# Kernel optimization log

Hardware: AMD Instinct MI355X
Metric: run time of the kernel (lower is better)

The kernel has to match this reference:

```python
import jax, jax.numpy as jnp
import numpy as np

B, N, D = 8, 65536, 3
K = 64                 # num_centers
NPOINT = 4096
M = NPOINT // K * 2    # max_neighbors = 128
S = NPOINT // K        # fps samples per group = 64
NITER = 10             # KMeans default Niter


def _sqdist(src, dst):
    # ||s||^2 + ||d||^2 - 2 s.d   (same math as (s-d)^2 sum, GEMM form)
    s2 = (src ** 2).sum(-1)[:, :, None]          # [B,N,1]
    d2 = (dst ** 2).sum(-1)[:, None, :]          # [B,1,K]
    return s2 + d2 - 2.0 * jnp.einsum('bnd,bkd->bnk', src, dst)


def _kmeans(x):
    Bb, Nn, Dd = x.shape
    c = x[:, :K, :]
    bidx = jnp.arange(Bb)[:, None]               # broadcast with cl [B,N]
    for _ in range(NITER):
        cl = jnp.argmin(_sqdist(x, c), axis=2)   # [B,N] cluster codes
        c = jnp.zeros((Bb, K, Dd), x.dtype).at[bidx, cl].add(x)
        ncl = jnp.zeros((Bb, K), x.dtype).at[bidx, cl].add(1.0)
        c = c / ncl[:, :, None]
    return c


def _query_neighbor(x, centers):
    dist = _sqdist(x, centers)                   # [B,N,K]
    negd = -jnp.transpose(dist, (0, 2, 1))       # [B,K,N]
    _, nidx = jax.lax.top_k(negd, M)             # M nearest points per center
    bidx = jnp.arange(x.shape[0])[:, None, None]
    return x[bidx, nidx]                         # [B,K,M,3]


def _batch_fps(xyz, farthest0):
    # xyz: [B,G,Nn,3]; sequential farthest-point sampling per group
    Bb, G, Nn, _ = xyz.shape
    dist0 = jnp.full((Bb, G, Nn), 1e10, xyz.dtype)

    def step(carry, _):
        distance, farthest = carry
        centroid = jnp.take_along_axis(xyz, farthest[:, :, None, None], axis=2)  # [B,G,1,3]
        d = ((xyz - centroid) ** 2).sum(-1)       # [B,G,Nn]
        distance = jnp.minimum(distance, d)
        new_far = jnp.argmax(distance, -1).astype(farthest.dtype)
        return (distance, new_far), farthest      # store index BEFORE update

    _, idx = jax.lax.scan(step, (dist0, farthest0), None, length=S)
    idx = jnp.transpose(idx, (1, 2, 0))           # [B,G,S]
    idx3 = jnp.broadcast_to(idx[..., None], idx.shape + (3,))
    new_xyz = jnp.take_along_axis(xyz, idx3, axis=2)  # [B,G,S,3]
    return new_xyz.reshape(Bb, G * S, 3)


def setup_inputs() -> dict:
    key = jax.random.key(0)
    k1, k2 = jax.random.split(key)
    x = jax.random.normal(k1, (B, N, D), dtype=jnp.float32)
    farthest0 = jax.random.randint(k2, (B, K), 0, M, dtype=jnp.int32)
    return {"x": x, "farthest0": farthest0}


def reference(x, farthest0):
    centers = _kmeans(x)                  # [B,K,3]
    neighbor = _query_neighbor(x, centers)  # [B,K,M,3]
    new_xyz = _batch_fps(neighbor, farthest0)  # [B, NPOINT, 3]
    return new_xyz, centers
```

## Files before the change

### kernel.cpp

```cpp
#include <hip/hip_runtime.h>
#include <stdint.h>

#pragma clang fp contract(off)

#define B 8
#define N 65536
#define KC 64
#define M 128
#define S 64
#define NITER 10
#define NWAVES 16
#define HPAD 257
#define SAMPLE 8192
#define SCAP 2048
#define CAPG 3072
#define WCAP 512
#define CSTRIDE 32
#define UPD_T 1024
#define RANGE 16384
#define NRANGE (N / RANGE)
#define PPT (RANGE / UPD_T)
#define GBATCH 2048

using u32 = unsigned int;
using u64 = unsigned long long;

__device__ __forceinline__ float sq3(float a, float b, float c) {
  return __fadd_rn(__fadd_rn(__fmul_rn(a, a), __fmul_rn(b, b)), __fmul_rn(c, c));
}
__device__ __forceinline__ float dot3(float x0, float x1, float x2,
                                      float c0, float c1, float c2) {
  return __fadd_rn(__fadd_rn(__fmul_rn(x0, c0), __fmul_rn(x1, c1)), __fmul_rn(x2, c2));
}
__device__ __forceinline__ float distf(float s2, float d2, float dt) {
  return __fsub_rn(__fadd_rn(s2, d2), __fmul_rn(2.0f, dt));
}
__device__ __forceinline__ u32 fkey(float f) {
  u32 u = __float_as_uint(f);
  return (u & 0x80000000u) ? ~u : (u | 0x80000000u);
}


__global__ void k_init_centers(const float* __restrict__ x, float* __restrict__ centers) {
  int i = blockIdx.x * blockDim.x + threadIdx.x;
  if (i >= B * KC * 3) return;
  int b = i / (KC * 3);
  int r = i % (KC * 3);
  centers[i] = x[(size_t)b * N * 3 + r];
}

__global__ __launch_bounds__(256)
void k_assign(const float* __restrict__ x, const float* __restrict__ centers,
              unsigned char* __restrict__ cl) {
  __shared__ float4 cs[KC];
  int g = blockIdx.x;
  int b = g & 7;
  int chunk = g >> 3;
  int t = threadIdx.x;
  if (t < KC) {
    float a0 = centers[(b * KC + t) * 3 + 0];
    float a1 = centers[(b * KC + t) * 3 + 1];
    float a2 = centers[(b * KC + t) * 3 + 2];
    cs[t] = make_float4(a0, a1, a2, sq3(a0, a1, a2));
  }
  __syncthreads();
  int q = chunk * 256 + t;
  const float4* xb4 = (const float4*)(x + (size_t)b * N * 3);
  float4 A = xb4[3 * q], Bv = xb4[3 * q + 1], C = xb4[3 * q + 2];
  float p0x = A.x, p0y = A.y, p0z = A.z;
  float p1x = A.w, p1y = Bv.x, p1z = Bv.y;
  float p2x = Bv.z, p2y = Bv.w, p2z = C.x;
  float p3x = C.y, p3y = C.z, p3z = C.w;
  float s0 = sq3(p0x, p0y, p0z);
  float s1 = sq3(p1x, p1y, p1z);
  float s2 = sq3(p2x, p2y, p2z);
  float s3 = sq3(p3x, p3y, p3z);
  float inf = __int_as_float(0x7f800000);
  float b0 = inf, b1 = inf, b2 = inf, b3 = inf;
  int i0 = 0, i1 = 0, i2 = 0, i3 = 0;
  for (int k = 0; k < KC; ++k) {
    float4 cc = cs[k];
    float d0 = distf(s0, cc.w, dot3(p0x, p0y, p0z, cc.x, cc.y, cc.z));
    float d1 = distf(s1, cc.w, dot3(p1x, p1y, p1z, cc.x, cc.y, cc.z));
    float d2 = distf(s2, cc.w, dot3(p2x, p2y, p2z, cc.x, cc.y, cc.z));
    float d3 = distf(s3, cc.w, dot3(p3x, p3y, p3z, cc.x, cc.y, cc.z));
    if (d0 < b0) { b0 = d0; i0 = k; }
    if (d1 < b1) { b1 = d1; i1 = k; }
    if (d2 < b2) { b2 = d2; i2 = k; }
    if (d3 < b3) { b3 = d3; i3 = k; }
  }
  *(u32*)(cl + (size_t)b * N + 4 * q) =
      (u32)i0 | ((u32)i1 << 8) | ((u32)i2 << 16) | ((u32)i3 << 24);
}

__global__ __launch_bounds__(UPD_T)
void k_cluster_update(const float* __restrict__ x, const unsigned char* __restrict__ cl,
                      float* __restrict__ centers) {
  __shared__ unsigned short midx[RANGE];
  __shared__ float bcoord[3][GBATCH + 1];
  __shared__ int woff[NWAVES];
  __shared__ int sCnt;
  int g = blockIdx.x;
  int bk = ((g & 7) << 6) | (g >> 3);
  int b = bk >> 6, k = bk & 63;
  int t = threadIdx.x, lane = t & 63, wid = t >> 6;
  const unsigned char* clb = cl + (size_t)b * N;
  const float* xb = x + (size_t)b * N * 3;
  float acc = 0.f;
  int cntAll = 0;

  for (int r = 0; r < NRANGE; ++r) {
    const uint4* cp = (const uint4*)(clb + r * RANGE);
    uint4 v = cp[t];
    u32 wsv[4] = {v.x, v.y, v.z, v.w};
    int m = 0;
#pragma unroll
    for (int j = 0; j < PPT; ++j)
      m += (((wsv[j >> 2] >> ((j & 3) * 8)) & 255u) == (u32)k);
    int incl = m;
#pragma unroll
    for (int o = 1; o < 64; o <<= 1) {
      int u = __shfl_up(incl, o);
      if (lane >= o) incl += u;
    }
    if (lane == 63) woff[wid] = incl;
    __syncthreads();
    if (t == 0) {
      int run = 0;
      for (int w = 0; w < NWAVES; ++w) { int vv = woff[w]; woff[w] = run; run += vv; }
      sCnt = run;
    }
    __syncthreads();
    int off = woff[wid] + incl - m;
    int mcnt = sCnt;
    int base = t * PPT;
#pragma unroll
    for (int j = 0; j < PPT; ++j) {
      if (((wsv[j >> 2] >> ((j & 3) * 8)) & 255u) == (u32)k)
        midx[off++] = (unsigned short)(base + j);
    }
    __syncthreads();
    for (int bo = 0; bo < mcnt; bo += GBATCH) {
      int bn = min(GBATCH, mcnt - bo);
      for (int i = t; i < bn; i += UPD_T) {
        int li = midx[bo + i];
        size_t src = ((size_t)(r * RANGE + li)) * 3;
        bcoord[0][i] = xb[src];
        bcoord[1][i] = xb[src + 1];
        bcoord[2][i] = xb[src + 2];
      }
      __syncthreads();
      if (wid == 0 && lane < 3) {
        const float* mb = &bcoord[lane][0];
#pragma unroll 8
        for (int i = 0; i < bn; ++i) acc = __fadd_rn(acc, mb[i]);
      }
      __syncthreads();
    }
    cntAll += mcnt;
    __syncthreads();
  }
  if (wid == 0 && lane < 3)
    centers[bk * 3 + lane] = __fdiv_rn(acc, (float)cntAll);
}

__global__ __launch_bounds__(256)
void k_thresh(const float* __restrict__ x, const float* __restrict__ centers,
              u32* __restrict__ thr, u32* __restrict__ cnt) {
  __shared__ u32 whist[4 * HPAD];
  __shared__ int sv[256];
  __shared__ u32 skeys[SCAP];
  __shared__ float4 scen;
  __shared__ u32 sSel;
  __shared__ int sNeed, sCntBin, sNum;
  int g = blockIdx.x;
  int bk = ((g & 7) << 6) | (g >> 3);
  int b = bk >> 6;
  int t = threadIdx.x, wid = t >> 6;
  if (t == 0) {
    float c0 = centers[bk * 3], c1 = centers[bk * 3 + 1], c2 = centers[bk * 3 + 2];
    scen = make_float4(c0, c1, c2, sq3(c0, c1, c2));
    cnt[bk * CSTRIDE] = 0;
    sNum = 0;
  }
  for (int i = t; i < 4 * HPAD; i += 256) whist[i] = 0;
  __syncthreads();
  float c0 = scen.x, c1 = scen.y, c2 = scen.z, d2 = scen.w;
  const float2* xb2 = (const float2*)(x + (size_t)b * N * 3);

  for (int p = t; p < SAMPLE / 2; p += 256) {
    float2 A = xb2[3 * p], Bv = xb2[3 * p + 1], C = xb2[3 * p + 2];
    float d0 = distf(sq3(A.x, A.y, Bv.x), d2, dot3(A.x, A.y, Bv.x, c0, c1, c2));
    float d1 = distf(sq3(Bv.y, C.x, C.y), d2, dot3(Bv.y, C.x, C.y, c0, c1, c2));
    atomicAdd(&whist[wid * HPAD + (fkey(d0) >> 24)], 1u);
    atomicAdd(&whist[wid * HPAD + (fkey(d1) >> 24)], 1u);
  }
  __syncthreads();
  int own = (int)(whist[0 * HPAD + t] + whist[1 * HPAD + t] +
                  whist[2 * HPAD + t] + whist[3 * HPAD + t]);
  sv[t] = own;
  __syncthreads();
  for (int off = 1; off < 256; off <<= 1) {
    int add = (t >= off) ? sv[t - off] : 0;
    __syncthreads();
    sv[t] += add;
    __syncthreads();
  }
  if (sv[t] >= M && sv[t] - own < M) {
    sSel = (u32)t; sNeed = M - (sv[t] - own); sCntBin = own;
  }
  __syncthreads();
  u32 selByte = sSel;
  int need = sNeed;
  int cntBin = sCntBin;
  u32 prefix = selByte << 24;

  if (cntBin <= SCAP) {
    for (int p = t; p < SAMPLE / 2; p += 256) {
      float2 A = xb2[3 * p], Bv = xb2[3 * p + 1], C = xb2[3 * p + 2];
      float d0 = distf(sq3(A.x, A.y, Bv.x), d2, dot3(A.x, A.y, Bv.x, c0, c1, c2));
      float d1 = distf(sq3(Bv.y, C.x, C.y), d2, dot3(Bv.y, C.x, C.y, c0, c1, c2));
      u32 k0 = fkey(d0), k1 = fkey(d1);
      if ((k0 >> 24) == selByte) skeys[atomicAdd(&sNum, 1)] = k0;
      if ((k1 >> 24) == selByte) skeys[atomicAdd(&sNum, 1)] = k1;
    }
    __syncthreads();
    int ne = sNum;
    for (int sh = 16; sh >= 0; sh -= 8) {
      whist[t] = 0;
      __syncthreads();
      for (int i = t; i < ne; i += 256) {
        u32 kk = skeys[i];
        if ((kk >> (sh + 8)) == (prefix >> (sh + 8)))
          atomicAdd(&whist[(kk >> sh) & 255u], 1u);
      }
      __syncthreads();
      int own2 = (int)whist[t];
      sv[t] = own2;
      __syncthreads();
      for (int off = 1; off < 256; off <<= 1) {
        int add = (t >= off) ? sv[t - off] : 0;
        __syncthreads();
        sv[t] += add;
        __syncthreads();
      }
      if (sv[t] >= need && sv[t] - own2 < need) {
        sSel = prefix | ((u32)t << sh);
        sNeed = need - (sv[t] - own2);
      }
      __syncthreads();
      prefix = sSel; need = sNeed;
      __syncthreads();
    }
    if (t == 0) thr[bk] = prefix;
  } else {
    if (t == 0) thr[bk] = prefix | 0x00FFFFFFu;
  }
}

__global__ __launch_bounds__(256)
void k_scatter_test(const float* __restrict__ x, const float* __restrict__ centers,
                    const u32* __restrict__ thr, u32* __restrict__ cnt,
                    u32* __restrict__ cand) {
  __shared__ float4 cs[KC];
  __shared__ u32 lthr[KC];
  __shared__ u64 wm0[4][KC], wm1[4][KC];
  __shared__ u32 wbase[4][KC];
  int g = blockIdx.x;
  int b = g & 7;
  int chunk = g >> 3;
  int t = threadIdx.x, lane = t & 63, wid = t >> 6;
  if (t < KC) {
    float a0 = centers[(b * KC + t) * 3 + 0];
    float a1 = centers[(b * KC + t) * 3 + 1];
    float a2 = centers[(b * KC + t) * 3 + 2];
    cs[t] = make_float4(a0, a1, a2, sq3(a0, a1, a2));
    lthr[t] = thr[b * KC + t];
  }
  __syncthreads();
  int pr = chunk * 256 + t;
  const float2* xb2 = (const float2*)(x + (size_t)b * N * 3);
  float2 A = xb2[3 * pr], Bv = xb2[3 * pr + 1], C = xb2[3 * pr + 2];
  float s20 = sq3(A.x, A.y, Bv.x);
  float s21 = sq3(Bv.y, C.x, C.y);
  u32 n0 = 2 * pr, n1 = 2 * pr + 1;
  u64 ltm = ((u64)1 << lane) - 1;

  for (int k = 0; k < KC; ++k) {
    float4 cc = cs[k];
    float d0 = distf(s20, cc.w, dot3(A.x, A.y, Bv.x, cc.x, cc.y, cc.z));
    float d1 = distf(s21, cc.w, dot3(Bv.y, C.x, C.y, cc.x, cc.y, cc.z));
    u64 m0 = __ballot(fkey(d0) <= lthr[k]);
    u64 m1 = __ballot(fkey(d1) <= lthr[k]);
    if (lane == 0) { wm0[wid][k] = m0; wm1[wid][k] = m1; }
  }
  __syncthreads();
  if (t < KC) {
    u32 pc[4];
    u32 total = 0;
#pragma unroll
    for (int w = 0; w < 4; ++w) {
      pc[w] = (u32)(__popcll(wm0[w][t]) + __popcll(wm1[w][t]));
      total += pc[w];
    }
    u32 base = (total > 0) ? atomicAdd(&cnt[(b * KC + t) * CSTRIDE], total) : 0u;
#pragma unroll
    for (int w = 0; w < 4; ++w) { wbase[w][t] = base; base += pc[w]; }
  }
  __syncthreads();
  u64 mybit = (u64)1 << lane;
  for (int k = 0; k < KC; ++k) {
    u64 m0 = wm0[wid][k], m1 = wm1[wid][k];
    if ((m0 | m1) == 0) continue;
    u32 wb = wbase[wid][k];
    u32* cb = cand + (size_t)(b * KC + k) * CAPG;
    if (m0 & mybit) {
      u32 pos = wb + (u32)__popcll(m0 & ltm);
      if (pos < CAPG) cb[pos] = n0;
    }
    if (m1 & mybit) {
      u32 pos = wb + (u32)__popcll(m0) + (u32)__popcll(m1 & ltm);
      if (pos < CAPG) cb[pos] = n1;
    }
  }
}

__global__ __launch_bounds__(256)
void k_topk_sort(const float* __restrict__ x, const float* __restrict__ centers,
                 const u32* __restrict__ cnt, const u32* __restrict__ cand,
                 float* __restrict__ neighbor) {
  __shared__ u64 candList[CAPG];
  __shared__ u32 hist[256];
  __shared__ u64 wbuf[WCAP];
  __shared__ u64 lessList[M];
  __shared__ u32 eqList[256];
  __shared__ u32 sSel;
  __shared__ int sNeed;
  __shared__ int cntW, cntLess, cntEq;
  __shared__ float4 scen;
  int g = blockIdx.x;
  int bk = ((g & 7) << 6) | (g >> 3);
  int b = bk >> 6;
  int t = threadIdx.x, lane = t & 63, wid = t >> 6;
  if (t == 0) {
    float c0 = centers[bk * 3], c1 = centers[bk * 3 + 1], c2 = centers[bk * 3 + 2];
    scen = make_float4(c0, c1, c2, sq3(c0, c1, c2));
    cntW = 0;
  }
  __syncthreads();
  float c0 = scen.x, c1 = scen.y, c2 = scen.z, d2 = scen.w;
  const float* xb = x + (size_t)b * N * 3;
  int cc = (int)cnt[bk * CSTRIDE];

  if (cc <= CAPG) {
    const u32* cb = cand + (size_t)bk * CAPG;
    for (int i = t; i < cc; i += 256) {
      u32 n = cb[i];
      float x0 = xb[n * 3], x1 = xb[n * 3 + 1], x2 = xb[n * 3 + 2];
      float d = distf(sq3(x0, x1, x2), d2, dot3(x0, x1, x2, c0, c1, c2));
      candList[i] = ((u64)fkey(d) << 32) | n;
    }
    __syncthreads();
    u32 prefix = 0;
    int need = M;
    for (int r = 3; r >= 0; --r) {
      int sh = r * 8;
      hist[t] = 0;
      __syncthreads();
      for (int i = t; i < cc; i += 256) {
        u32 key = (u32)(candList[i] >> 32);
        bool ok = (r == 3) || ((key >> (sh + 8)) == (prefix >> (sh + 8)));
        if (ok) atomicAdd(&hist[(key >> sh) & 255u], 1u);
      }
      __syncthreads();
      if (wid == 0) {
        u32 h0 = hist[4 * lane + 0], h1 = hist[4 * lane + 1];
        u32 h2 = hist[4 * lane + 2], h3 = hist[4 * lane + 3];
        u32 lsum = h0 + h1 + h2 + h3;
        u32 incl = lsum;
#pragma unroll
        for (int o = 1; o < 64; o <<= 1) {
          u32 u = __shfl_up(incl, o);
          if (lane >= o) incl += u;
        }
        u32 excl = incl - lsum;
        if ((int)excl < need && need <= (int)incl) {
          u32 hh[4] = {h0, h1, h2, h3};
          u32 cum = excl; int bin = -1; u32 bc = 0;
#pragma unroll
          for (int j = 0; j < 4; ++j) {
            if (bin < 0 && (int)(cum + hh[j]) >= need) { bin = 4 * lane + j; bc = cum; }
            cum += hh[j];
          }
          sSel = prefix | ((u32)bin << sh);
          sNeed = need - (int)bc;
        }
      }
      __syncthreads();
      prefix = sSel; need = sNeed;
      __syncthreads();
    }
    u32 K128 = prefix;
    for (int i = t; i < cc; i += 256) {
      u64 e = candList[i];
      if ((u32)(e >> 32) <= K128) {
        int p = atomicAdd(&cntW, 1);
        if (p < WCAP) wbuf[p] = e;
      }
    }
    __syncthreads();
    int wcnt = cntW;
    if (wcnt <= WCAP) {
      for (int i = t; i < WCAP; i += 256) if (i >= wcnt) wbuf[i] = ~0ull;
      __syncthreads();
      for (int ksz = 2; ksz <= WCAP; ksz <<= 1) {
        for (int j = ksz >> 1; j > 0; j >>= 1) {
          for (int idx = t; idx < WCAP; idx += 256) {
            int ixj = idx ^ j;
            if (ixj > idx) {
              u64 a = wbuf[idx], bb = wbuf[ixj];
              bool up = ((idx & ksz) == 0);
              if (up ? (a > bb) : (a < bb)) { wbuf[idx] = bb; wbuf[ixj] = a; }
            }
          }
          __syncthreads();
        }
      }
      if (t < M) {
        int idx = (int)(wbuf[t] & 0xFFFFFFFFu);
        size_t src = ((size_t)b * N + idx) * 3;
        size_t dst = ((size_t)bk * M + t) * 3;
        neighbor[dst]     = x[src];
        neighbor[dst + 1] = x[src + 1];
        neighbor[dst + 2] = x[src + 2];
      }
      return;
    }
  }

  if (t == 0) { cntLess = 0; cntEq = 0; }
  __syncthreads();
  u32 prefix = 0;
  int need = M;
  for (int r = 3; r >= 0; --r) {
    for (int i = t; i < 256; i += 256) hist[i] = 0;
    __syncthreads();
    int sh = r * 8;
    for (int n = t; n < N; n += 256) {
      float x0 = xb[n * 3], x1 = xb[n * 3 + 1], x2 = xb[n * 3 + 2];
      float d = distf(sq3(x0, x1, x2), d2, dot3(x0, x1, x2, c0, c1, c2));
      u32 key = fkey(d);
      bool ok = (r == 3) || ((key >> (sh + 8)) == (prefix >> (sh + 8)));
      if (ok) atomicAdd(&hist[(key >> sh) & 255u], 1u);
    }
    __syncthreads();
    if (t == 0) {
      int cum = 0;
      for (int bin = 0; bin < 256; ++bin) {
        int c = (int)hist[bin];
        if (cum + c >= need) { sSel = prefix | ((u32)bin << sh); sNeed = need - cum; break; }
        cum += c;
      }
    }
    __syncthreads();
    prefix = sSel; need = sNeed;
    __syncthreads();
  }
  u32 K128 = prefix;

  for (int n = t; n < N; n += 256) {
    float x0 = xb[n * 3], x1 = xb[n * 3 + 1], x2 = xb[n * 3 + 2];
    float d = distf(sq3(x0, x1, x2), d2, dot3(x0, x1, x2, c0, c1, c2));
    u32 key = fkey(d);
    if (key < K128) {
      int p = atomicAdd(&cntLess, 1);
      if (p < M) lessList[p] = ((u64)key << 32) | (u32)n;
    } else if (key == K128) {
      int p = atomicAdd(&cntEq, 1);
      if (p < 256) eqList[p] = (u32)n;
    }
  }
  __syncthreads();
  int nl = cntLess;
  int ne2 = cntEq;
  for (int i = t; i < M; i += 256) if (i >= nl) lessList[i] = ~0ull;
  for (int i = t; i < 256; i += 256) if (i >= ne2) eqList[i] = 0xFFFFFFFFu;
  __syncthreads();

  for (int ksz = 2; ksz <= M; ksz <<= 1) {
    for (int j = ksz >> 1; j > 0; j >>= 1) {
      for (int idx = t; idx < M; idx += 256) {
        int ixj = idx ^ j;
        if (ixj > idx) {
          u64 a = lessList[idx], bb = lessList[ixj];
          bool up = ((idx & ksz) == 0);
          if (up ? (a > bb) : (a < bb)) { lessList[idx] = bb; lessList[ixj] = a; }
        }
      }
      __syncthreads();
    }
  }
  for (int ksz = 2; ksz <= 256; ksz <<= 1) {
    for (int j = ksz >> 1; j > 0; j >>= 1) {
      for (int idx = t; idx < 256; idx += 256) {
        int ixj = idx ^ j;
        if (ixj > idx) {
          u32 a = eqList[idx], bb = eqList[ixj];
          bool up = ((idx & ksz) == 0);
          if (up ? (a > bb) : (a < bb)) { eqList[idx] = bb; eqList[ixj] = a; }
        }
      }
      __syncthreads();
    }
  }

  if (t < M) {
    int idx = (t < nl) ? (int)(lessList[t] & 0xFFFFFFFFu) : (int)eqList[t - nl];
    size_t src = ((size_t)b * N + idx) * 3;
    size_t dst = ((size_t)bk * M + t) * 3;
    neighbor[dst]     = x[src];
    neighbor[dst + 1] = x[src + 1];
    neighbor[dst + 2] = x[src + 2];
  }
}

__global__ void k_fps(const float* __restrict__ neighbor, const int* __restrict__ farthest0,
                      const float* __restrict__ centers, float* __restrict__ out) {
  __shared__ float px[M], py[M], pz[M];
  __shared__ float wv[2];
  __shared__ int wi[2];
  int bg = blockIdx.x;
  int b = bg >> 6, g = bg & 63;
  int t = threadIdx.x;
  {
    int i = bg * 128 + t;
    if (i < B * KC * 3) out[B * 4096 * 3 + i] = centers[i];
  }
  size_t src = ((size_t)bg * M + t) * 3;
  float mx = neighbor[src], my = neighbor[src + 1], mz = neighbor[src + 2];
  px[t] = mx; py[t] = my; pz[t] = mz;
  int far = farthest0[bg];
  float dist = 1e10f;
  __syncthreads();
  for (int s = 0; s < S; ++s) {
    if (t == far) {
      size_t dst = ((size_t)b * 4096 + g * 64 + s) * 3;
      out[dst] = mx; out[dst + 1] = my; out[dst + 2] = mz;
    }
    float cx = px[far], cy = py[far], cz = pz[far];
    float dx = __fsub_rn(mx, cx), dy = __fsub_rn(my, cy), dz = __fsub_rn(mz, cz);
    float d = sq3(dx, dy, dz);
    dist = fminf(dist, d);
    float v = dist;
    int i = t;
#pragma unroll
    for (int off = 1; off < 64; off <<= 1) {
      float ov = __shfl_xor(v, off);
      int oi = __shfl_xor(i, off);
      if (ov > v || (ov == v && oi < i)) { v = ov; i = oi; }
    }
    int wid = t >> 6;
    if ((t & 63) == 0) { wv[wid] = v; wi[wid] = i; }
    __syncthreads();
    float v0 = wv[0]; int i0 = wi[0];
    float v1 = wv[1]; int i1 = wi[1];
    far = (v1 > v0 || (v1 == v0 && i1 < i0)) ? i1 : i0;
    __syncthreads();
  }
}

extern "C" void kernel_launch(void* const* d_in, const int* in_sizes, int n_in,
                              void* d_out, int out_size, void* d_ws, size_t ws_size,
                              hipStream_t stream) {
  const float* x = (const float*)d_in[0];
  const int* farthest0 = (const int*)d_in[1];
  float* out = (float*)d_out;

  char* w = (char*)d_ws;
  float* centers         = (float*)(w);
  unsigned char* cl      = (unsigned char*)(w + 8192);
  u32* thr               = (u32*)(w + 8192 + 524288);
  u32* cnt               = (u32*)(w + 8192 + 524288 + 4096);
  float* neighbor        = (float*)(w + 8192 + 524288 + 4096 + 65536);
  u32* cand              = (u32*)(w + 8192 + 524288 + 4096 + 65536 + 786432);

  k_init_centers<<<6, 256, 0, stream>>>(x, centers);
  for (int it = 0; it < NITER; ++it) {
    k_assign<<<B * 64, 256, 0, stream>>>(x, centers, cl);
    k_cluster_update<<<B * KC, UPD_T, 0, stream>>>(x, cl, centers);
  }
  k_thresh<<<B * KC, 256, 0, stream>>>(x, centers, thr, cnt);
  k_scatter_test<<<B * 128, 256, 0, stream>>>(x, centers, thr, cnt, cand);
  k_topk_sort<<<B * KC, 256, 0, stream>>>(x, centers, cnt, cand, neighbor);
  k_fps<<<B * KC, M, 0, stream>>>(neighbor, farthest0, centers, out);
}
```

Measured before the change: 500.4 us.

## Run FPS in a single wave with packed 64-bit argmax keys

```diff
diff --git a/kernel.cpp b/kernel.cpp
--- a/kernel.cpp
+++ b/kernel.cpp
@@ -524,48 +524,45 @@
   }
 }
 
-__global__ void k_fps(const float* __restrict__ neighbor, const int* __restrict__ farthest0,
-                      const float* __restrict__ centers, float* __restrict__ out) {
-  __shared__ float px[M], py[M], pz[M];
-  __shared__ float wv[2];
-  __shared__ int wi[2];
+__global__ __launch_bounds__(64)
+void k_fps(const float* __restrict__ neighbor, const int* __restrict__ farthest0,
+           const float* __restrict__ centers, float* __restrict__ out) {
+  __shared__ float4 pts[M];
   int bg = blockIdx.x;
   int b = bg >> 6, g = bg & 63;
   int t = threadIdx.x;
   {
-    int i = bg * 128 + t;
+    int i = bg * 64 + t;
     if (i < B * KC * 3) out[B * 4096 * 3 + i] = centers[i];
   }
-  size_t src = ((size_t)bg * M + t) * 3;
-  float mx = neighbor[src], my = neighbor[src + 1], mz = neighbor[src + 2];
-  px[t] = mx; py[t] = my; pz[t] = mz;
+  const float* nb = neighbor + (size_t)bg * M * 3;
+  float ax = nb[6 * t],     ay = nb[6 * t + 1], az = nb[6 * t + 2];
+  float bx = nb[6 * t + 3], by = nb[6 * t + 4], bz = nb[6 * t + 5];
+  pts[2 * t]     = make_float4(ax, ay, az, 0.f);
+  pts[2 * t + 1] = make_float4(bx, by, bz, 0.f);
   int far = farthest0[bg];
-  float dist = 1e10f;
-  __syncthreads();
+  float dist0 = 1e10f, dist1 = 1e10f;
+  __syncthreads();
+  float* ob = out + ((size_t)b * 4096 + g * 64) * 3;
   for (int s = 0; s < S; ++s) {
-    if (t == far) {
-      size_t dst = ((size_t)b * 4096 + g * 64 + s) * 3;
-      out[dst] = mx; out[dst + 1] = my; out[dst + 2] = mz;
-    }
-    float cx = px[far], cy = py[far], cz = pz[far];
-    float dx = __fsub_rn(mx, cx), dy = __fsub_rn(my, cy), dz = __fsub_rn(mz, cz);
-    float d = sq3(dx, dy, dz);
-    dist = fminf(dist, d);
-    float v = dist;
-    int i = t;
+    if ((far >> 1) == t) {
+      if (far & 1) { ob[3 * s] = bx; ob[3 * s + 1] = by; ob[3 * s + 2] = bz; }
+      else         { ob[3 * s] = ax; ob[3 * s + 1] = ay; ob[3 * s + 2] = az; }
+    }
+    float4 cc = pts[far];
+    float d0 = sq3(__fsub_rn(ax, cc.x), __fsub_rn(ay, cc.y), __fsub_rn(az, cc.z));
+    float d1 = sq3(__fsub_rn(bx, cc.x), __fsub_rn(by, cc.y), __fsub_rn(bz, cc.z));
+    dist0 = fminf(dist0, d0);
+    dist1 = fminf(dist1, d1);
+    u64 k0 = ((u64)__float_as_uint(dist0) << 32) | (u32)(M - 1 - 2 * t);
+    u64 k1 = ((u64)__float_as_uint(dist1) << 32) | (u32)(M - 2 - 2 * t);
+    u64 key = (k0 > k1) ? k0 : k1;
 #pragma unroll
     for (int off = 1; off < 64; off <<= 1) {
-      float ov = __shfl_xor(v, off);
-      int oi = __shfl_xor(i, off);
-      if (ov > v || (ov == v && oi < i)) { v = ov; i = oi; }
-    }
-    int wid = t >> 6;
-    if ((t & 63) == 0) { wv[wid] = v; wi[wid] = i; }
-    __syncthreads();
-    float v0 = wv[0]; int i0 = wi[0];
-    float v1 = wv[1]; int i1 = wi[1];
-    far = (v1 > v0 || (v1 == v0 && i1 < i0)) ? i1 : i0;
-    __syncthreads();
+      u64 o = __shfl_xor(key, off);
+      if (o > key) key = o;
+    }
+    far = M - 1 - (int)(key & 0xFFFFFFFFu);
   }
 }
 
@@ -592,5 +589,5 @@
   k_thresh<<<B * KC, 256, 0, stream>>>(x, centers, thr, cnt);
   k_scatter_test<<<B * 128, 256, 0, stream>>>(x, centers, thr, cnt, cand);
   k_topk_sort<<<B * KC, 256, 0, stream>>>(x, centers, cnt, cand, neighbor);
-  k_fps<<<B * KC, M, 0, stream>>>(neighbor, farthest0, centers, out);
-}
+  k_fps<<<B * KC, M / 2, 0, stream>>>(neighbor, farthest0, centers, out);
+}
```

Result: faster. 483.1 us (-3.5%).
